# Kernel tuning notes

Hardware: AMD Instinct MI355X
Metric: run time of the kernel (lower is better)

## Reference

```python
import jax, jax.numpy as jnp
import numpy as np

M = 7
EPS = 1e-8

def setup_inputs() -> dict:
    key = jax.random.key(0)
    ks = jax.random.split(key, 6)
    B, C, H, W = 8, 256, 128, 128
    return {
        "x": jax.random.normal(ks[0], (B, C, H, W), dtype=jnp.float32),
        "w1": jax.random.normal(ks[1], (M * M, 32), dtype=jnp.float32) * 0.1,
        "b1": jnp.zeros((32,), dtype=jnp.float32),
        "w2": jax.random.normal(ks[2], (32, 3), dtype=jnp.float32) * 0.1,
        "b2": jnp.zeros((3,), dtype=jnp.float32),
        "wr": jax.random.normal(ks[3], (256, 256), dtype=jnp.float32) * (1.0 / 16.0),
    }

def _aniso_kernels(params):
    # params: [B,3] -> normalized anisotropic Gaussian kernels [B,M,M]
    theta = jnp.arctan2(params[:, 0], params[:, 1]) / 2.0 + jnp.pi / 2.0
    lam1 = jnp.exp(params[:, 2])
    lam2 = 1.0 / (lam1 + EPS)
    lin = jnp.linspace(-(M // 2), M // 2, M, dtype=params.dtype)
    yy, xx = jnp.meshgrid(lin, lin, indexing="ij")  # matches torch.meshgrid 'ij'
    cos_t = jnp.cos(theta)[:, None, None]
    sin_t = jnp.sin(theta)[:, None, None]
    x_rot = xx * cos_t + yy * sin_t
    y_rot = -xx * sin_t + yy * cos_t
    k = jnp.exp(-(x_rot ** 2 / (2.0 * lam1[:, None, None] ** 2)
                  + y_rot ** 2 / (2.0 * lam2[:, None, None] ** 2)))
    return k / (k.sum(axis=(1, 2), keepdims=True) + EPS)

def reference(x, w1, b1, w2, b2, wr):
    B, C, H, W = x.shape
    xf = jnp.fft.fftshift(jnp.fft.fft2(x, norm="ortho"), axes=(-2, -1))
    # center m x m crop of channel-mean magnitude
    mag = jnp.abs(xf).mean(axis=1)  # [B,H,W]
    h0, w0 = H // 2 - M // 2, W // 2 - M // 2
    center = mag[:, h0:h0 + M, w0:w0 + M].reshape(B, M * M)
    hid = jax.nn.relu(center @ w1 + b1)
    params = hid @ w2 + b2  # [B,3]
    kern = _aniso_kernels(params)  # [B,M,M], shared across channels per sample
    # depthwise filtering: one 7x7 kernel per sample applied to all 2C (real|imag) channels
    stacked = jnp.concatenate([xf.real, xf.imag], axis=1)  # [B,2C,H,W]
    pad = [(M // 2, M // 2)] * 2
    def conv_one(img, k):  # img [2C,H,W], k [M,M]
        return jax.lax.conv_general_dilated(img[:, None], k[None, None],
                                            (1, 1), pad)[:, 0]
    filt = jax.vmap(conv_one)(stacked, kern)  # [B,2C,H,W]
    real_f, imag_f = filt[:, :C], filt[:, C:]
    rr = jnp.einsum("bchw,oc->bohw", real_f, wr)  # refine_conv 1x1, no bias
    ii = jnp.einsum("bchw,oc->bohw", imag_f, wr)
    out_f = jnp.fft.ifftshift(jax.lax.complex(rr, ii), axes=(-2, -1))
    return jnp.fft.ifft2(out_f, norm="ortho").real + x
```

## Files before the change

kernel.cpp:

```cpp
#include <hip/hip_runtime.h>

#define HW 16384
#define PIf 3.14159265358979323846f
typedef unsigned short ushortt;
typedef unsigned int uint32;
typedef __attribute__((ext_vector_type(8))) short short8;
typedef __attribute__((ext_vector_type(4))) float f32x4;
typedef __attribute__((ext_vector_type(2))) float f32x2;
typedef __attribute__((ext_vector_type(2))) unsigned int uintv2;

__device__ __forceinline__ float bf2f(ushortt b) {
    return __uint_as_float(((unsigned)b) << 16);
}
__device__ __forceinline__ ushortt f2bf(float f) {
    unsigned u = __float_as_uint(f);
    u += 0x7fffu + ((u >> 16) & 1u);
    return (ushortt)(u >> 16);
}
__device__ __forceinline__ int brev6(int v) { return (int)(__brev((unsigned)v) >> 26); }

__device__ __forceinline__ void bfly(float& Ar, float& Ai, float& Br, float& Bi,
                                     float tr, float ti) {
    float sr = Ar + Br, si = Ai + Bi;
    float dr = Ar - Br, di = Ai - Bi;
    Ar = sr; Ai = si;
    Br = dr * tr - di * ti;
    Bi = dr * ti + di * tr;
}

__device__ __forceinline__ void xswap32(float& a, float& b) {
    uintv2 r = __builtin_amdgcn_permlane32_swap(__float_as_uint(a), __float_as_uint(b), false, false);
    a = __uint_as_float(r.x); b = __uint_as_float(r.y);
}
__device__ __forceinline__ void xswap16(float& a, float& b) {
    uintv2 r = __builtin_amdgcn_permlane16_swap(__float_as_uint(a), __float_as_uint(b), false, false);
    a = __uint_as_float(r.x); b = __uint_as_float(r.y);
}
template<int IMM>
__device__ __forceinline__ void pswap_sw(float& a, float& b, bool up) {
    float sel = up ? a : b;
    float rcv = __int_as_float(__builtin_amdgcn_ds_swizzle(__float_as_int(sel), IMM));
    a = up ? rcv : a;
    b = up ? b : rcv;
}
template<int CTRL>
__device__ __forceinline__ void pswap_dpp(float& a, float& b, bool up) {
    float sel = up ? a : b;
    float rcv = __int_as_float(__builtin_amdgcn_update_dpp(0, __float_as_int(sel), CTRL, 0xF, 0xF, true));
    a = up ? rcv : a;
    b = up ? b : rcv;
}

struct TwSet { float r0,i0,r1,i1,r2,i2,r3,i3,r4,i4,r5,i5; };

__device__ __forceinline__ TwSet load_tw(const float* __restrict__ twr,
                                         const float* __restrict__ twi, int l) {
    TwSet t;
    t.r0 = twr[l];            t.i0 = twi[l];
    t.r1 = twr[(l & 31) << 1]; t.i1 = twi[(l & 31) << 1];
    t.r2 = twr[(l & 15) << 2]; t.i2 = twi[(l & 15) << 2];
    t.r3 = twr[(l & 7)  << 3]; t.i3 = twi[(l & 7)  << 3];
    t.r4 = twr[(l & 3)  << 4]; t.i4 = twi[(l & 3)  << 4];
    t.r5 = twr[(l & 1)  << 5]; t.i5 = twi[(l & 1)  << 5];
    return t;
}

__device__ __forceinline__ void fft128_ps(float& Ar, float& Ai, float& Br, float& Bi,
                                          const TwSet& t,
                                          bool u8, bool u4, bool u2, bool u1) {
    bfly(Ar, Ai, Br, Bi, t.r0, t.i0);
    xswap32(Ar, Br); xswap32(Ai, Bi);
    bfly(Ar, Ai, Br, Bi, t.r1, t.i1);
    xswap16(Ar, Br); xswap16(Ai, Bi);
    bfly(Ar, Ai, Br, Bi, t.r2, t.i2);
    pswap_sw<0x201F>(Ar, Br, u8); pswap_sw<0x201F>(Ai, Bi, u8);
    bfly(Ar, Ai, Br, Bi, t.r3, t.i3);
    pswap_sw<0x101F>(Ar, Br, u4); pswap_sw<0x101F>(Ai, Bi, u4);
    bfly(Ar, Ai, Br, Bi, t.r4, t.i4);
    pswap_dpp<0x4E>(Ar, Br, u2); pswap_dpp<0x4E>(Ai, Bi, u2);
    bfly(Ar, Ai, Br, Bi, t.r5, t.i5);
    pswap_dpp<0xB1>(Ar, Br, u1); pswap_dpp<0xB1>(Ai, Bi, u1);
    {
        float sr = Ar + Br, si = Ai + Bi;
        float dr = Ar - Br, di = Ai - Bi;
        Ar = sr; Ai = si; Br = dr; Bi = di;
    }
}

__global__ __launch_bounds__(1024) void fft_fwd(const float* __restrict__ x,
                                                ushortt* __restrict__ xfRe,
                                                ushortt* __restrict__ xfIm,
                                                float* __restrict__ magc) {
    __shared__ float2 sc[128][129];
    __shared__ float twr[64], twi[64];
    int img = blockIdx.x;
    int tid = threadIdx.x, l = tid & 63, wv = tid >> 6;
    if (tid < 64) {
        float s, c;
        sincosf(-PIf * (float)tid / 64.0f, &s, &c);
        twr[tid] = c; twi[tid] = s;
    }
    const float* xi = x + (size_t)img * HW;
    __syncthreads();

    TwSet t = load_tw(twr, twi, l);
    bool u8 = (l & 8) != 0, u4 = (l & 4) != 0, u2 = (l & 2) != 0, u1 = (l & 1) != 0;
    int e = brev6(l);

    float nar = xi[(wv * 8) * 128 + l];
    float nbr = xi[(wv * 8) * 128 + 64 + l];
    for (int r = 0; r < 8; ++r) {
        int row = wv * 8 + r;
        float Ar = nar, Ai = 0.f, Br = nbr, Bi = 0.f;
        if (r < 7) {
            nar = xi[(row + 1) * 128 + l];
            nbr = xi[(row + 1) * 128 + 64 + l];
        }
        fft128_ps(Ar, Ai, Br, Bi, t, u8, u4, u2, u1);
        sc[row][e]      = make_float2(Ar, Ai);
        sc[row][e + 64] = make_float2(Br, Bi);
    }
    __syncthreads();

    for (int r = 0; r < 8; ++r) {
        int c = wv * 8 + r;
        float2 va = sc[l][c], vb = sc[l + 64][c];
        float Ar = va.x, Ai = va.y, Br = vb.x, Bi = vb.y;
        fft128_ps(Ar, Ai, Br, Bi, t, u8, u4, u2, u1);
        sc[e][c]      = make_float2(Ar, Ai);
        sc[e + 64][c] = make_float2(Br, Bi);
    }
    __syncthreads();

    uint32* oRe = (uint32*)(xfRe + ((size_t)img << 14));
    uint32* oIm = (uint32*)(xfIm + ((size_t)img << 14));
    for (int idx2 = tid; idx2 < 8192; idx2 += 1024) {
        int p = idx2 >> 6, qp = idx2 & 63, q = qp * 2;
        int u  = (p + 64) & 127;
        int v0 = (q + 64) & 127;
        const float scl = 1.0f / 128.0f;
        float2 e0 = sc[u][v0], e1 = sc[u][v0 + 1];
        uint32 re = (uint32)f2bf(e0.x * scl) | ((uint32)f2bf(e1.x * scl) << 16);
        uint32 im = (uint32)f2bf(e0.y * scl) | ((uint32)f2bf(e1.y * scl) << 16);
        oRe[p * 64 + qp] = re;
        oIm[p * 64 + qp] = im;
    }
    if (tid < 49) {
        int p = 61 + tid / 7, q = 61 + tid % 7;
        int u = (p + 64) & 127, v = (q + 64) & 127;
        float2 z = sc[u][v];
        float mag = sqrtf(z.x * z.x + z.y * z.y) * (1.0f / 128.0f);
        atomicAdd(&magc[(img >> 8) * 49 + tid], mag);
    }
}

__global__ __launch_bounds__(256) void mlp_kern(const float* __restrict__ magc,
                                                const float* __restrict__ w1,
                                                const float* __restrict__ b1,
                                                const float* __restrict__ w2,
                                                const float* __restrict__ b2,
                                                float2* __restrict__ kern_pk) {
    __shared__ float hid[8][32];
    __shared__ float par[8][3];
    __shared__ float kun[8][49];
    __shared__ float ksum[8];
    int tid = threadIdx.x;
    {
        int b = tid >> 5, n = tid & 31;
        float acc = b1[n];
        for (int i = 0; i < 49; ++i)
            acc = fmaf(magc[b * 49 + i] * (1.0f / 256.0f), w1[i * 32 + n], acc);
        hid[b][n] = fmaxf(acc, 0.f);
    }
    __syncthreads();
    if (tid < 24) {
        int b = tid / 3, j = tid % 3;
        float acc = b2[j];
        for (int n = 0; n < 32; ++n) acc = fmaf(hid[b][n], w2[n * 3 + j], acc);
        par[b][j] = acc;
    }
    __syncthreads();
    for (int idx = tid; idx < 392; idx += 256) {
        int b = idx / 49, ij = idx % 49;
        int i = ij / 7, j2 = ij % 7;
        float p0 = par[b][0], p1 = par[b][1], p2 = par[b][2];
        float theta = atan2f(p0, p1) * 0.5f + PIf * 0.5f;
        float lam1 = expf(p2);
        float lam2 = 1.0f / (lam1 + 1e-8f);
        float yy = (float)(i - 3), xx = (float)(j2 - 3);
        float ct, st;
        sincosf(theta, &st, &ct);
        float xr =  xx * ct + yy * st;
        float yr = -xx * st + yy * ct;
        kun[b][ij] = expf(-(xr * xr / (2.f * lam1 * lam1) + yr * yr / (2.f * lam2 * lam2)));
    }
    __syncthreads();
    if (tid < 8) {
        float s = 0.f;
        for (int t = 0; t < 49; ++t) s += kun[tid][t];
        ksum[tid] = s + 1e-8f;
    }
    __syncthreads();
    for (int idx = tid; idx < 448; idx += 256) {
        int b  = idx / 56;
        int r7 = idx - b * 56;
        int rr = r7 / 7, dx = r7 - rr * 7;
        float inv = 1.0f / ksum[b];
        float v0 = (rr < 7)  ? kun[b][rr * 7 + dx] * inv       : 0.f;
        float v1 = (rr >= 1) ? kun[b][(rr - 1) * 7 + dx] * inv : 0.f;
        kern_pk[idx] = make_float2(v0, v1);
    }
}

__global__ __launch_bounds__(256) void gemm_mix(const ushortt* __restrict__ xfRe,
                                                const ushortt* __restrict__ xfIm,
                                                const float* __restrict__ wr,
                                                ushortt* __restrict__ mixRe,
                                                ushortt* __restrict__ mixIm) {
    __shared__ ushortt lA[2][5120];
    __shared__ uint32  lB[2][2560];
    int tid = threadIdx.x;
    int lane = tid & 63, wave = tid >> 6;
    int wm = wave >> 1, wn = wave & 1;
    int l15 = lane & 15, q4 = lane >> 4;
    int b = blockIdx.z >> 1, part = blockIdx.z & 1;
    const ushortt* Xb = (part ? xfIm : xfRe) + (size_t)b * (256 * HW)
                        + blockIdx.x * 128;
    ushortt* Dst = (part ? mixIm : mixRe) + (size_t)b * (256 * HW)
                   + (size_t)(blockIdx.y * 128) * HW + blockIdx.x * 128;
    const float* W = wr + (blockIdx.y * 128) * 256;

    int srow = tid >> 1, shalf = tid & 1;
    const float* wRow = W + srow * 256 + shalf * 16;
    int ldsOffA = srow * 40 + shalf * 16;

    int kt = tid >> 4;
    int pq = tid & 15;
    int kswz = kt ^ ((pq & 3) << 2);
    int rowbase = pq * 160;

    float4 wreg[4];
    uint4  a0, a1;
    #pragma unroll
    for (int i = 0; i < 4; ++i) wreg[i] = *(const float4*)(wRow + i * 4);
    {
        const ushortt* xp = Xb + (size_t)(2 * kt) * HW + pq * 8;
        a0 = *(const uint4*)xp;
        a1 = *(const uint4*)(xp + HW);
    }

    f32x4 acc[4][4];
    #pragma unroll
    for (int i = 0; i < 4; ++i)
        #pragma unroll
        for (int j = 0; j < 4; ++j)
            #pragma unroll
            for (int k = 0; k < 4; ++k) acc[i][j][k] = 0.f;

    int abase = (wm * 64 + l15) * 40 + q4 * 8;
    int baddr[4];
    #pragma unroll
    for (int f = 0; f < 4; ++f) {
        int pf = wn * 64 + f * 16 + l15;
        baddr[f] = pf * 40 + ((q4 ^ ((pf >> 3) & 3)) << 3);
    }

    for (int kb = 0; kb < 8; ++kb) {
        int bufc = kb & 1;
        {
            float ff[16] = {wreg[0].x, wreg[0].y, wreg[0].z, wreg[0].w,
                            wreg[1].x, wreg[1].y, wreg[1].z, wreg[1].w,
                            wreg[2].x, wreg[2].y, wreg[2].z, wreg[2].w,
                            wreg[3].x, wreg[3].y, wreg[3].z, wreg[3].w};
            uint32 p[8];
            #pragma unroll
            for (int j = 0; j < 8; ++j)
                p[j] = (uint32)f2bf(ff[2 * j]) | ((uint32)f2bf(ff[2 * j + 1]) << 16);
            *(uint4*)&lA[bufc][ldsOffA]     = make_uint4(p[0], p[1], p[2], p[3]);
            *(uint4*)&lA[bufc][ldsOffA + 8] = make_uint4(p[4], p[5], p[6], p[7]);
        }
        {
            uint32 d[8];
            d[0] = (a0.x & 0xffffu) | (a1.x << 16);
            d[1] = (a0.x >> 16)     | (a1.x & 0xffff0000u);
            d[2] = (a0.y & 0xffffu) | (a1.y << 16);
            d[3] = (a0.y >> 16)     | (a1.y & 0xffff0000u);
            d[4] = (a0.z & 0xffffu) | (a1.z << 16);
            d[5] = (a0.z >> 16)     | (a1.z & 0xffff0000u);
            d[6] = (a0.w & 0xffffu) | (a1.w << 16);
            d[7] = (a0.w >> 16)     | (a1.w & 0xffff0000u);
            uint32* lb = lB[bufc];
            #pragma unroll
            for (int j = 0; j < 8; ++j) lb[rowbase + j * 20 + kswz] = d[j];
        }
        __syncthreads();
        if (kb < 7) {
            const float* wN = wRow + (kb + 1) * 32;
            #pragma unroll
            for (int i = 0; i < 4; ++i) wreg[i] = *(const float4*)(wN + i * 4);
            const ushortt* xp = Xb + (size_t)((kb + 1) * 32 + 2 * kt) * HW + pq * 8;
            a0 = *(const uint4*)xp;
            a1 = *(const uint4*)(xp + HW);
        }
        short8 af[4], bf[4];
        const ushortt* lbU = (const ushortt*)lB[bufc];
        #pragma unroll
        for (int f = 0; f < 4; ++f) af[f] = *(const short8*)&lA[bufc][abase + f * 640];
        #pragma unroll
        for (int f = 0; f < 4; ++f) bf[f] = *(const short8*)&lbU[baddr[f]];
        #pragma unroll
        for (int fi = 0; fi < 4; ++fi)
            #pragma unroll
            for (int fj = 0; fj < 4; ++fj)
                acc[fi][fj] = __builtin_amdgcn_mfma_f32_16x16x32_bf16(
                    af[fi], bf[fj], acc[fi][fj], 0, 0, 0);
    }
    #pragma unroll
    for (int fi = 0; fi < 4; ++fi) {
        #pragma unroll
        for (int r = 0; r < 4; ++r) {
            int o_l = wm * 64 + fi * 16 + q4 * 4 + r;
            ushortt* dp = Dst + (size_t)o_l * HW + wn * 64 + l15;
            #pragma unroll
            for (int fj = 0; fj < 4; ++fj)
                dp[fj * 16] = f2bf(acc[fi][fj][r]);
        }
    }
}

__global__ __launch_bounds__(256) void conv7(const ushortt* __restrict__ mixRe,
                                             const ushortt* __restrict__ mixIm,
                                             const float2* __restrict__ kern_pk,
                                             ushortt* __restrict__ outRe,
                                             ushortt* __restrict__ outIm) {
    __shared__ float tile[70 * 74];
    int b = blockIdx.z;
    int plane = blockIdx.y;
    int part = plane >> 8;
    size_t pbase = ((size_t)(b * 256 + (plane & 255))) << 14;
    const ushortt* src = (part ? mixIm : mixRe) + pbase;
    ushortt* dst = (part ? outIm : outRe) + pbase;
    int ty = (blockIdx.x >> 1) * 64, tx = (blockIdx.x & 1) * 64;
    int tid = threadIdx.x;
    const float2* kp = kern_pk + b * 56;

    for (int idx = tid; idx < 2520; idx += 256) {
        int row = idx / 36, du = idx - row * 36;
        int gy = ty + row - 3, gx0 = tx - 4 + 2 * du;
        uint32 v = 0u;
        if ((unsigned)gy < 128u && (unsigned)gx0 < 128u)
            v = *(const uint32*)(src + gy * 128 + gx0);
        float2 w;
        w.x = __uint_as_float(v << 16);
        w.y = __uint_as_float(v & 0xffff0000u);
        *(float2*)&tile[row * 74 + 2 * du] = w;
    }
    __syncthreads();

    int ox = (tid & 7) * 8, oy = (tid >> 3) * 2;
    f32x2 acc2[8];
    #pragma unroll
    for (int j = 0; j < 8; ++j) { acc2[j].x = 0.f; acc2[j].y = 0.f; }

    #pragma unroll
    for (int dyy = 0; dyy < 8; ++dyy) {
        float row[14];
        #pragma unroll
        for (int m = 0; m < 14; ++m) row[m] = tile[(oy + dyy) * 74 + ox + 1 + m];
        #pragma unroll
        for (int dx = 0; dx < 7; ++dx) {
            float2 kl = kp[dyy * 7 + dx];
            f32x2 kk; kk.x = kl.x; kk.y = kl.y;
            #pragma unroll
            for (int j = 0; j < 8; ++j) {
                f32x2 rr; rr.x = row[dx + j]; rr.y = row[dx + j];
                acc2[j] = __builtin_elementwise_fma(rr, kk, acc2[j]);
            }
        }
    }

    uint32 s0[4], s1[4];
    #pragma unroll
    for (int m = 0; m < 4; ++m) {
        s0[m] = (uint32)f2bf(acc2[2 * m].x) | ((uint32)f2bf(acc2[2 * m + 1].x) << 16);
        s1[m] = (uint32)f2bf(acc2[2 * m].y) | ((uint32)f2bf(acc2[2 * m + 1].y) << 16);
    }
    *(uint4*)(dst + (ty + oy) * 128 + tx + ox)     = make_uint4(s0[0], s0[1], s0[2], s0[3]);
    *(uint4*)(dst + (ty + oy + 1) * 128 + tx + ox) = make_uint4(s1[0], s1[1], s1[2], s1[3]);
}

__global__ __launch_bounds__(1024) void ifft_add(const ushortt* __restrict__ convRe,
                                                 const ushortt* __restrict__ convIm,
                                                 const float* __restrict__ x,
                                                 float* __restrict__ out) {
    __shared__ float2 sc[128][129];
    __shared__ float twr[64], twi[64];
    int img = blockIdx.x;
    int tid = threadIdx.x, l = tid & 63, wv = tid >> 6;
    if (tid < 64) {
        float s, c;
        sincosf(-PIf * (float)tid / 64.0f, &s, &c);
        twr[tid] = c; twi[tid] = s;
    }
    const ushortt* cr = convRe + ((size_t)img << 14);
    const ushortt* ci = convIm + ((size_t)img << 14);
    __syncthreads();

    TwSet t = load_tw(twr, twi, l);
    bool u8 = (l & 8) != 0, u4 = (l & 4) != 0, u2 = (l & 2) != 0, u1 = (l & 1) != 0;
    int e = brev6(l);

    {
        int p0 = ((wv * 8) + 64) & 127;
        float nar = bf2f(cr[p0 * 128 + 64 + l]), nai = bf2f(ci[p0 * 128 + 64 + l]);
        float nbr = bf2f(cr[p0 * 128 + l]),      nbi = bf2f(ci[p0 * 128 + l]);
        for (int r = 0; r < 8; ++r) {
            int u = wv * 8 + r;
            float Ar = nar, Ai = -nai, Br = nbr, Bi = -nbi;
            if (r < 7) {
                int p = ((u + 1) + 64) & 127;
                nar = bf2f(cr[p * 128 + 64 + l]); nai = bf2f(ci[p * 128 + 64 + l]);
                nbr = bf2f(cr[p * 128 + l]);      nbi = bf2f(ci[p * 128 + l]);
            }
            fft128_ps(Ar, Ai, Br, Bi, t, u8, u4, u2, u1);
            sc[u][e]      = make_float2(Ar, Ai);
            sc[u][e + 64] = make_float2(Br, Bi);
        }
    }
    __syncthreads();

    for (int r = 0; r < 8; ++r) {
        int c = wv * 8 + r;
        float2 va = sc[l][c], vbv = sc[l + 64][c];
        float Ar = va.x, Ai = va.y, Br = vbv.x, Bi = vbv.y;
        fft128_ps(Ar, Ai, Br, Bi, t, u8, u4, u2, u1);
        sc[e][c]      = make_float2(Ar, Ai);
        sc[e + 64][c] = make_float2(Br, Bi);
    }
    __syncthreads();

    const float* xi = x + (size_t)img * HW;
    float* oo = out + (size_t)img * HW;
    for (int idx2 = tid; idx2 < 8192; idx2 += 1024) {
        int y = idx2 >> 6, xp = (idx2 & 63) * 2;
        float r0 = sc[y][xp].x     * (1.0f / 128.0f);
        float r1 = sc[y][xp + 1].x * (1.0f / 128.0f);
        float2 xv = *(const float2*)(xi + y * 128 + xp);
        float2 ov; ov.x = r0 + xv.x; ov.y = r1 + xv.y;
        *(float2*)(oo + y * 128 + xp) = ov;
    }
}

extern "C" void kernel_launch(void* const* d_in, const int* in_sizes, int n_in,
                              void* d_out, int out_size, void* d_ws, size_t ws_size,
                              hipStream_t stream) {
    const float* x  = (const float*)d_in[0];
    const float* w1 = (const float*)d_in[1];
    const float* b1 = (const float*)d_in[2];
    const float* w2 = (const float*)d_in[3];
    const float* b2 = (const float*)d_in[4];
    const float* wr = (const float*)d_in[5];

    char* ws = (char*)d_ws;
    ushortt* xfRe  = (ushortt*)ws;
    ushortt* xfIm  = xfRe + 33554432;
    ushortt* mixRe = (ushortt*)(ws + 134217728);
    ushortt* mixIm = mixRe + 33554432;
    ushortt* convRe = xfRe, *convIm = xfIm;
    float* magc = (float*)(ws + 268435456);
    float2* kern_pk = (float2*)(ws + 268435456 + 2048);

    hipMemsetAsync(magc, 0, 392 * sizeof(float), stream);
    fft_fwd<<<2048, 1024, 0, stream>>>(x, xfRe, xfIm, magc);
    mlp_kern<<<1, 256, 0, stream>>>(magc, w1, b1, w2, b2, kern_pk);
    gemm_mix<<<dim3(128, 2, 16), 256, 0, stream>>>(xfRe, xfIm, wr, mixRe, mixIm);
    conv7<<<dim3(4, 512, 8), 256, 0, stream>>>(mixRe, mixIm, kern_pk, convRe, convIm);
    ifft_add<<<2048, 1024, 0, stream>>>(convRe, convIm, x, (float*)d_out);
}
```

Measured before the change: 595.8 us.

## Exploit real-signal symmetry: pack row pairs into complex FFTs in forward and inverse

The forward 2D FFT now packs two real rows into one complex 128-point FFT and separates them through Hermitian symmetry in the column pass. The inverse FFT likewise packs two real output columns into one complex transform, which halves the column-pass FFT work. Scale factors move to 1/256 to absorb the packing factor of two. This cuts butterfly arithmetic and LDS traffic in the two FFT kernels, but adds extra shared-memory gathers, an additional barrier and more register arrays, which may raise register pressure.

```diff
diff --git a/kernel.cpp b/kernel.cpp
--- a/kernel.cpp
+++ b/kernel.cpp
@@ -107,28 +107,46 @@
     bool u8 = (l & 8) != 0, u4 = (l & 4) != 0, u2 = (l & 2) != 0, u1 = (l & 1) != 0;
     int e = brev6(l);
 
-    float nar = xi[(wv * 8) * 128 + l];
-    float nbr = xi[(wv * 8) * 128 + 64 + l];
+    float lar[4], lai[4], lbr[4], lbi[4];
+    #pragma unroll
+    for (int r = 0; r < 4; ++r) {
+        int p = wv * 4 + r;
+        lar[r] = xi[(2 * p) * 128 + l];
+        lai[r] = xi[(2 * p + 1) * 128 + l];
+        lbr[r] = xi[(2 * p) * 128 + 64 + l];
+        lbi[r] = xi[(2 * p + 1) * 128 + 64 + l];
+    }
+    #pragma unroll
+    for (int r = 0; r < 4; ++r) {
+        int p = wv * 4 + r;
+        float Ar = lar[r], Ai = lai[r], Br = lbr[r], Bi = lbi[r];
+        fft128_ps(Ar, Ai, Br, Bi, t, u8, u4, u2, u1);
+        sc[p][e]      = make_float2(Ar, Ai);
+        sc[p][e + 64] = make_float2(Br, Bi);
+    }
+    __syncthreads();
+
+    float oar[8], oai[8], obr[8], obi[8];
+    int pa = l >> 1, pb = 32 + (l >> 1);
+    bool odd = (l & 1) != 0;
+    #pragma unroll
     for (int r = 0; r < 8; ++r) {
-        int row = wv * 8 + r;
-        float Ar = nar, Ai = 0.f, Br = nbr, Bi = 0.f;
-        if (r < 7) {
-            nar = xi[(row + 1) * 128 + l];
-            nbr = xi[(row + 1) * 128 + 64 + l];
-        }
+        int c = wv * 8 + r, cm = (128 - c) & 127;
+        float2 Za = sc[pa][c], Zma = sc[pa][cm];
+        float2 Zb = sc[pb][c], Zmb = sc[pb][cm];
+        float Ar = odd ? (Za.y + Zma.y) : (Za.x + Zma.x);
+        float Ai = odd ? (Zma.x - Za.x) : (Za.y - Zma.y);
+        float Br = odd ? (Zb.y + Zmb.y) : (Zb.x + Zmb.x);
+        float Bi = odd ? (Zmb.x - Zb.x) : (Zb.y - Zmb.y);
         fft128_ps(Ar, Ai, Br, Bi, t, u8, u4, u2, u1);
-        sc[row][e]      = make_float2(Ar, Ai);
-        sc[row][e + 64] = make_float2(Br, Bi);
-    }
-    __syncthreads();
-
+        oar[r] = Ar; oai[r] = Ai; obr[r] = Br; obi[r] = Bi;
+    }
+    __syncthreads();
+    #pragma unroll
     for (int r = 0; r < 8; ++r) {
         int c = wv * 8 + r;
-        float2 va = sc[l][c], vb = sc[l + 64][c];
-        float Ar = va.x, Ai = va.y, Br = vb.x, Bi = vb.y;
-        fft128_ps(Ar, Ai, Br, Bi, t, u8, u4, u2, u1);
-        sc[e][c]      = make_float2(Ar, Ai);
-        sc[e + 64][c] = make_float2(Br, Bi);
+        sc[e][c]      = make_float2(oar[r], oai[r]);
+        sc[e + 64][c] = make_float2(obr[r], obi[r]);
     }
     __syncthreads();
 
@@ -138,7 +156,7 @@
         int p = idx2 >> 6, qp = idx2 & 63, q = qp * 2;
         int u  = (p + 64) & 127;
         int v0 = (q + 64) & 127;
-        const float scl = 1.0f / 128.0f;
+        const float scl = 1.0f / 256.0f;
         float2 e0 = sc[u][v0], e1 = sc[u][v0 + 1];
         uint32 re = (uint32)f2bf(e0.x * scl) | ((uint32)f2bf(e1.x * scl) << 16);
         uint32 im = (uint32)f2bf(e0.y * scl) | ((uint32)f2bf(e1.y * scl) << 16);
@@ -149,7 +167,7 @@
         int p = 61 + tid / 7, q = 61 + tid % 7;
         int u = (p + 64) & 127, v = (q + 64) & 127;
         float2 z = sc[u][v];
-        float mag = sqrtf(z.x * z.x + z.y * z.y) * (1.0f / 128.0f);
+        float mag = sqrtf(z.x * z.x + z.y * z.y) * (1.0f / 256.0f);
         atomicAdd(&magc[(img >> 8) * 49 + tid], mag);
     }
 }
@@ -411,17 +429,19 @@
     int e = brev6(l);
 
     {
-        int p0 = ((wv * 8) + 64) & 127;
-        float nar = bf2f(cr[p0 * 128 + 64 + l]), nai = bf2f(ci[p0 * 128 + 64 + l]);
-        float nbr = bf2f(cr[p0 * 128 + l]),      nbi = bf2f(ci[p0 * 128 + l]);
+        float nar[8], nai[8], nbr[8], nbi[8];
+        #pragma unroll
+        for (int r = 0; r < 8; ++r) {
+            int p = ((wv * 8 + r) + 64) & 127;
+            nar[r] = bf2f(cr[p * 128 + 64 + l]);
+            nai[r] = bf2f(ci[p * 128 + 64 + l]);
+            nbr[r] = bf2f(cr[p * 128 + l]);
+            nbi[r] = bf2f(ci[p * 128 + l]);
+        }
+        #pragma unroll
         for (int r = 0; r < 8; ++r) {
             int u = wv * 8 + r;
-            float Ar = nar, Ai = -nai, Br = nbr, Bi = -nbi;
-            if (r < 7) {
-                int p = ((u + 1) + 64) & 127;
-                nar = bf2f(cr[p * 128 + 64 + l]); nai = bf2f(ci[p * 128 + 64 + l]);
-                nbr = bf2f(cr[p * 128 + l]);      nbi = bf2f(ci[p * 128 + l]);
-            }
+            float Ar = nar[r], Ai = -nai[r], Br = nbr[r], Bi = -nbi[r];
             fft128_ps(Ar, Ai, Br, Bi, t, u8, u4, u2, u1);
             sc[u][e]      = make_float2(Ar, Ai);
             sc[u][e + 64] = make_float2(Br, Bi);
@@ -429,25 +449,43 @@
     }
     __syncthreads();
 
-    for (int r = 0; r < 8; ++r) {
-        int c = wv * 8 + r;
-        float2 va = sc[l][c], vbv = sc[l + 64][c];
-        float Ar = va.x, Ai = va.y, Br = vbv.x, Bi = vbv.y;
+    float oar[4], oai[4], obr[4], obi[4];
+    int rv  = (128 - l) & 127;
+    int rv2 = (64 - l) & 127;
+    #pragma unroll
+    for (int r = 0; r < 4; ++r) {
+        int m = wv * 4 + r;
+        int c0 = 2 * m, c1 = 2 * m + 1;
+        float2 P  = sc[l][c0],      R  = sc[l][c1];
+        float2 Q  = sc[rv][c0],     S  = sc[rv][c1];
+        float2 P2 = sc[l + 64][c0], R2 = sc[l + 64][c1];
+        float2 Q2 = sc[rv2][c0],    S2 = sc[rv2][c1];
+        float Ar = P.x + Q.x - R.y + S.y;
+        float Ai = P.y - Q.y + R.x + S.x;
+        float Br = P2.x + Q2.x - R2.y + S2.y;
+        float Bi = P2.y - Q2.y + R2.x + S2.x;
         fft128_ps(Ar, Ai, Br, Bi, t, u8, u4, u2, u1);
-        sc[e][c]      = make_float2(Ar, Ai);
-        sc[e + 64][c] = make_float2(Br, Bi);
+        oar[r] = Ar; oai[r] = Ai; obr[r] = Br; obi[r] = Bi;
+    }
+    __syncthreads();
+    #pragma unroll
+    for (int r = 0; r < 4; ++r) {
+        int m = wv * 4 + r;
+        sc[e][m]      = make_float2(oar[r], oai[r]);
+        sc[e + 64][m] = make_float2(obr[r], obi[r]);
     }
     __syncthreads();
 
     const float* xi = x + (size_t)img * HW;
     float* oo = out + (size_t)img * HW;
     for (int idx2 = tid; idx2 < 8192; idx2 += 1024) {
-        int y = idx2 >> 6, xp = (idx2 & 63) * 2;
-        float r0 = sc[y][xp].x     * (1.0f / 128.0f);
-        float r1 = sc[y][xp + 1].x * (1.0f / 128.0f);
-        float2 xv = *(const float2*)(xi + y * 128 + xp);
-        float2 ov; ov.x = r0 + xv.x; ov.y = r1 + xv.y;
-        *(float2*)(oo + y * 128 + xp) = ov;
+        int y = idx2 >> 6, m = idx2 & 63;
+        float2 v = sc[y][m];
+        float2 xv = *(const float2*)(xi + y * 128 + 2 * m);
+        float2 ov;
+        ov.x = v.x * (1.0f / 256.0f) + xv.x;
+        ov.y = v.y * (1.0f / 256.0f) + xv.y;
+        *(float2*)(oo + y * 128 + 2 * m) = ov;
     }
 }
 
```

Result: faster. 579.2 us (-2.8%).
